# Optimization experiments

Hardware: AMD Instinct MI355X
Metric: run time of the kernel (lower is better)

Reference implementation:

```python
import jax, jax.numpy as jnp
import numpy as np

B, S, D = 2, 2048, 2048
H = 16
NOPE, ROPE, VDIM = 128, 64, 128
QKD = NOPE + ROPE  # 192
KV_RANK = 512
EPS = 1e-6
SCALE = QKD ** -0.5  # rope_factor <= 1.0 -> no mscale correction


def _rotate_half(x):
    h = x.shape[-1] // 2
    return jnp.concatenate([-x[..., h:], x[..., :h]], axis=-1)


def _rms_norm(x, w):
    var = jnp.mean(jnp.square(x), axis=-1, keepdims=True)
    return x * jax.lax.rsqrt(var + EPS) * w


def setup_inputs() -> dict:
    key = jax.random.key(0)
    ks = jax.random.split(key, 8)
    hidden_states = jax.random.normal(ks[0], (B, S, D), dtype=jnp.float32)
    cos = jax.random.uniform(ks[1], (S, ROPE), dtype=jnp.float32)
    sin = jax.random.uniform(ks[2], (S, ROPE), dtype=jnp.float32)
    # parameters (torch Linear stores [out, in]; keep same layout)
    wq_w = jax.random.normal(ks[3], (H * QKD, D), dtype=jnp.float32) * (D ** -0.5)
    wkv_a_w = jax.random.normal(ks[4], (KV_RANK + ROPE, D), dtype=jnp.float32) * (D ** -0.5)
    kv_norm_w = jnp.ones((KV_RANK,), dtype=jnp.float32)
    wkv_b_w = jax.random.normal(ks[5], (H * (NOPE + VDIM), KV_RANK), dtype=jnp.float32) * (KV_RANK ** -0.5)
    wo_w = jax.random.normal(ks[6], (D, H * VDIM), dtype=jnp.float32) * ((H * VDIM) ** -0.5)
    return dict(hidden_states=hidden_states, cos=cos, sin=sin,
                wq_w=wq_w, wkv_a_w=wkv_a_w, kv_norm_w=kv_norm_w,
                wkv_b_w=wkv_b_w, wo_w=wo_w)


def reference(hidden_states, cos, sin, wq_w, wkv_a_w, kv_norm_w, wkv_b_w, wo_w):
    x = hidden_states
    # q projection (q_lora_rank == 0 path)
    q = jnp.einsum('bsd,od->bso', x, wq_w).reshape(B, S, H, QKD)
    q_nope, q_pe = q[..., :NOPE], q[..., NOPE:]
    # low-rank kv
    kv_all = jnp.einsum('bsd,od->bso', x, wkv_a_w)  # [B,S,KV_RANK+ROPE]
    kv, k_pe = kv_all[..., :KV_RANK], kv_all[..., KV_RANK:]
    kv_proj = jnp.einsum('bsr,or->bso', _rms_norm(kv, kv_norm_w), wkv_b_w)
    kv_proj = kv_proj.reshape(B, S, H, NOPE + VDIM)
    k_nope, v = kv_proj[..., :NOPE], kv_proj[..., NOPE:]
    # rotary on pe parts; k_pe broadcast over heads
    c = cos[None, :, None, :]  # [1,S,1,ROPE]
    s = sin[None, :, None, :]
    q_pe = q_pe * c + _rotate_half(q_pe) * s
    k_pe_h = k_pe[:, :, None, :]  # broadcast over heads
    k_pe_h = k_pe_h * c + _rotate_half(k_pe_h) * s
    k_pe_h = jnp.broadcast_to(k_pe_h, (B, S, H, ROPE))
    k = jnp.concatenate([k_nope, k_pe_h], axis=-1)  # [B,S,H,QKD]
    qf = jnp.concatenate([q_nope, q_pe], axis=-1)
    # naive attention, fp32 softmax
    scores = jnp.einsum('bshd,bthd->bsht', qf, k) * SCALE
    attn = jax.nn.softmax(scores.astype(jnp.float32), axis=-1).astype(x.dtype)
    out = jnp.einsum('bsht,bthd->bshd', attn, v).reshape(B, S, H * VDIM)
    return jnp.einsum('bsf,of->bso', out, wo_w)
```

## Files before the change

kernel.cpp:

```cpp
#include <hip/hip_runtime.h>
#include <cstdint>


typedef _Float16 f16;
typedef _Float16 f16x8 __attribute__((ext_vector_type(8)));
typedef _Float16 f16x4 __attribute__((ext_vector_type(4)));
typedef float    f32x4 __attribute__((ext_vector_type(4)));

#define SCALE_L2E 0.104117550f

__device__ __forceinline__ void gl2lds16(const void* g, void* lds_wave_base) {
  __builtin_amdgcn_global_load_lds(
      (const __attribute__((address_space(1))) uint32_t*)(uintptr_t)g,
      (__attribute__((address_space(3))) uint32_t*)(uint32_t)(uintptr_t)lds_wave_base,
      16, 0, 0);
}

__global__ __launch_bounds__(256) void k_cvt(
    const float* __restrict__ x, const float* __restrict__ wq,
    const float* __restrict__ wkvb, const float* __restrict__ wo,
    const float* __restrict__ wkva,
    f16* __restrict__ xb, f16* __restrict__ wqb,
    f16* __restrict__ wkvbb, f16* __restrict__ wob,
    f16* __restrict__ wkvab)
{
  size_t i = ((size_t)blockIdx.x * 256 + threadIdx.x) * 4;
  if (i >= 20971520ull) {
    size_t il = i - 20971520ull;
    int r = (int)(il >> 11);
    f16x4 h;
    if (r < 576) {
      float4 v = *(const float4*)(wkva + il);
      h[0]=(f16)v.x; h[1]=(f16)v.y; h[2]=(f16)v.z; h[3]=(f16)v.w;
    } else { h[0]=h[1]=h[2]=h[3]=(f16)0.f; }
    *(f16x4*)(wkvab + il) = h;
    return;
  }
  const float* src; f16* dst; size_t off; float scl = 1.0f;
  if (i < 8388608ull)            { src = x;    dst = xb;    off = i; }
  else if (i < 14680064ull)      { src = wq;   dst = wqb;   off = i - 8388608ull; scl = SCALE_L2E; }
  else if (i < 16777216ull)      { src = wkvb; dst = wkvbb; off = i - 14680064ull; }
  else                           { src = wo;   dst = wob;   off = i - 16777216ull; }
  float4 v = *(const float4*)(src + off);
  f16x4 h; h[0]=(f16)(v.x*scl); h[1]=(f16)(v.y*scl); h[2]=(f16)(v.z*scl); h[3]=(f16)(v.w*scl);
  *(f16x4*)(dst + off) = h;
}

template<class Epi>
__device__ __forceinline__ void gemm256_core(const f16* __restrict__ Ablk,
                                             const f16* __restrict__ Bblk,
                                             int K, Epi epi)
{
  __shared__ __align__(16) f16 As[2][256 * 64];
  __shared__ __align__(16) f16 Bs[2][256 * 64];

  const int tid  = threadIdx.x;
  const int lane = tid & 63;
  const int wv   = tid >> 6;
  const int wm   = (wv >> 2) * 128;
  const int wn   = (wv & 3) * 64;
  const int lrow = lane & 15;
  const int lk   = lane >> 4;

  f32x4 acc[8][4];
#pragma unroll
  for (int i = 0; i < 8; ++i)
#pragma unroll
    for (int j = 0; j < 4; ++j) acc[i][j] = f32x4{0.f, 0.f, 0.f, 0.f};

  const int NT = K >> 6;

  const f16* aptr[4]; const f16* bptr[4]; int ldsbase[4];
#pragma unroll
  for (int q = 0; q < 4; ++q) {
    int s = q * 512 + tid;
    int r = s >> 3, c = s & 7;
    int gc = c ^ (r & 7);
    aptr[q] = Ablk + (size_t)r * K + gc * 8;
    bptr[q] = Bblk + (size_t)r * K + gc * 8;
    ldsbase[q] = (q * 512 + wv * 64) * 8;
  }

#pragma unroll
  for (int q = 0; q < 4; ++q) gl2lds16(aptr[q], (f16*)As[0] + ldsbase[q]);
#pragma unroll
  for (int q = 0; q < 4; ++q) gl2lds16(bptr[q], (f16*)Bs[0] + ldsbase[q]);

  for (int t = 0; t < NT; ++t) {
    const int cur = t & 1;
    asm volatile("s_waitcnt vmcnt(0)" ::: "memory");
    __builtin_amdgcn_s_barrier();
    const f16* Ac = As[cur];
    const f16* Bc = Bs[cur];
    const bool more = (t + 1 < NT);
    const int koff = (t + 1) * 64;
#pragma unroll
    for (int p = 0; p < 4; ++p) {
      if (p == 0 && more) {
#pragma unroll
        for (int q = 0; q < 4; ++q)
          gl2lds16(aptr[q] + koff, (f16*)As[cur ^ 1] + ldsbase[q]);
      }
      if (p == 1 && more) {
#pragma unroll
        for (int q = 0; q < 4; ++q)
          gl2lds16(bptr[q] + koff, (f16*)Bs[cur ^ 1] + ldsbase[q]);
      }
      const int mh = p >> 1, nh = p & 1;
      f16x8 af[2][4], bf[2][2];
#pragma unroll
      for (int ks = 0; ks < 2; ++ks) {
#pragma unroll
        for (int i = 0; i < 4; ++i) {
          int ra = wm + mh * 64 + i * 16 + lrow;
          int ca = (ks * 4 + lk) ^ (ra & 7);
          af[ks][i] = *(const f16x8*)(Ac + ra * 64 + ca * 8);
        }
#pragma unroll
        for (int j = 0; j < 2; ++j) {
          int rb = wn + nh * 32 + j * 16 + lrow;
          int cb = (ks * 4 + lk) ^ (rb & 7);
          bf[ks][j] = *(const f16x8*)(Bc + rb * 64 + cb * 8);
        }
      }
      __builtin_amdgcn_s_barrier();
      __builtin_amdgcn_s_setprio(1);
#pragma unroll
      for (int ks = 0; ks < 2; ++ks)
#pragma unroll
        for (int i = 0; i < 4; ++i)
#pragma unroll
          for (int j = 0; j < 2; ++j)
            acc[mh * 4 + i][nh * 2 + j] = __builtin_amdgcn_mfma_f32_16x16x32_f16(
                af[ks][i], bf[ks][j], acc[mh * 4 + i][nh * 2 + j], 0, 0, 0);
      __builtin_amdgcn_s_setprio(0);
      if (p < 3) __builtin_amdgcn_s_barrier();
    }
  }
  epi(acc, wm, wn, lk, lrow);
}

__global__ __launch_bounds__(512, 2) void k_gemm_qkva(
    const f16* __restrict__ xb, const f16* __restrict__ wqb,
    const f16* __restrict__ wkvab, const float* __restrict__ cosb,
    const float* __restrict__ sinb,
    f16* __restrict__ qraw, f16* __restrict__ kva)
{
  int nb = blockIdx.x, m0 = blockIdx.y * 256;
  bool isq = nb < 12;
  const f16* Bblk = isq ? wqb + (size_t)nb * 256 * 2048
                        : wkvab + (size_t)(nb - 12) * 256 * 2048;
  gemm256_core(xb + (size_t)m0 * 2048, Bblk, 2048,
    [&](f32x4 (&acc)[8][4], int wm, int wn, int lk, int lrow) {
      if (isq) {
        f16* Cb = qraw + (size_t)m0 * 3072 + nb * 256;
        int g = nb * 4 + (wn >> 6);
        if (g % 3 == 2) {
#pragma unroll
          for (int I = 0; I < 8; ++I)
#pragma unroll
            for (int rr = 0; rr < 4; ++rr) {
              int row = wm + I * 16 + lk * 4 + rr;
              int s = (m0 + row) & 2047;
              const float* cbp = cosb + (size_t)s * 64;
              const float* sbp = sinb + (size_t)s * 64;
#pragma unroll
              for (int J = 0; J < 4; ++J) {
                int tt = J * 16 + lrow;
                float v  = acc[I][J][rr];
                float pr = acc[I][J ^ 2][rr];
                float o = (J < 2) ? (v * cbp[tt] - pr * sbp[tt])
                                  : (v * cbp[tt] + pr * sbp[tt]);
                Cb[(size_t)row * 3072 + wn + J * 16 + lrow] = (f16)o;
              }
            }
          return;
        }
#pragma unroll
        for (int I = 0; I < 8; ++I)
#pragma unroll
          for (int rr = 0; rr < 4; ++rr) {
            int row = wm + I * 16 + lk * 4 + rr;
#pragma unroll
            for (int J = 0; J < 4; ++J)
              Cb[(size_t)row * 3072 + wn + J * 16 + lrow] = (f16)acc[I][J][rr];
          }
      } else {
        int n0k = (nb - 12) * 256;
        if (n0k + wn >= 640) return;
        f16* Cb = kva + (size_t)m0 * 640 + n0k;
#pragma unroll
        for (int I = 0; I < 8; ++I)
#pragma unroll
          for (int rr = 0; rr < 4; ++rr) {
            int row = wm + I * 16 + lk * 4 + rr;
#pragma unroll
            for (int J = 0; J < 4; ++J)
              Cb[(size_t)row * 640 + wn + J * 16 + lrow] = (f16)acc[I][J][rr];
          }
      }
    });
}

__global__ __launch_bounds__(512, 2) void k_gemm_kvb(
    const f16* __restrict__ kvn, const f16* __restrict__ wkvbb,
    f16* __restrict__ knope, f16* __restrict__ vf)
{
  int hh = blockIdx.x, m0 = blockIdx.y * 256;
  gemm256_core(kvn + (size_t)m0 * 512, wkvbb + (size_t)hh * 256 * 512, 512,
    [&](f32x4 (&acc)[8][4], int wm, int wn, int lk, int lrow) {
      if (wn >= 128) {
#pragma unroll
        for (int I = 0; I < 8; ++I) {
          int trow = m0 + wm + I * 16 + lk * 4;
          int bb = trow >> 11, ss = trow & 2047;
#pragma unroll
          for (int J = 0; J < 4; ++J) {
            int vd = (wn - 128) + J * 16 + lrow;
            f16x4 pk;
#pragma unroll
            for (int rr = 0; rr < 4; ++rr) pk[rr] = (f16)acc[I][J][rr];
            *(f16x4*)(vf + ((size_t)(bb * 16 + hh) * 128 + vd) * 2048 + ss) = pk;
          }
        }
      } else {
#pragma unroll
        for (int I = 0; I < 8; ++I)
#pragma unroll
          for (int rr = 0; rr < 4; ++rr) {
            int trow = m0 + wm + I * 16 + lk * 4 + rr;
#pragma unroll
            for (int J = 0; J < 4; ++J)
              knope[(size_t)trow * 2048 + hh * 128 + wn + J * 16 + lrow] = (f16)acc[I][J][rr];
          }
      }
    });
}

template<class Epi>
__device__ __forceinline__ void gemm_core(const f16* __restrict__ Ablk,
                                          const f16* __restrict__ Bblk,
                                          int K, Epi epi)
{
  __shared__ __align__(16) f16 As[128 * 64];
  __shared__ __align__(16) f16 Bs[128 * 64];

  const int tid  = threadIdx.x;
  const int lane = tid & 63;
  const int wv   = tid >> 6;
  const int wm = (wv >> 1) * 64, wn = (wv & 1) * 64;
  const int lrow = lane & 15;
  const int lk   = lane >> 4;

  f32x4 acc[4][4];
#pragma unroll
  for (int i = 0; i < 4; ++i)
#pragma unroll
    for (int j = 0; j < 4; ++j) acc[i][j] = f32x4{0.f, 0.f, 0.f, 0.f};

  for (int k0 = 0; k0 < K; k0 += 64) {
    __syncthreads();
#pragma unroll
    for (int it = 0; it < 4; ++it) {
      int s  = it * 256 + tid;
      int r  = s >> 3, sc = s & 7;
      int gc = sc ^ (r & 7);
      gl2lds16(Ablk + (size_t)r * K + k0 + gc * 8, (f16*)As + (size_t)(it * 256 + wv * 64) * 8);
      gl2lds16(Bblk + (size_t)r * K + k0 + gc * 8, (f16*)Bs + (size_t)(it * 256 + wv * 64) * 8);
    }
    __syncthreads();

#pragma unroll
    for (int ks = 0; ks < 2; ++ks) {
      f16x8 af[4], bf[4];
#pragma unroll
      for (int i = 0; i < 4; ++i) {
        int ra = wm + i * 16 + lrow;
        int ca = (ks * 4 + lk) ^ (ra & 7);
        af[i] = *(const f16x8*)(As + ra * 64 + ca * 8);
        int rb = wn + i * 16 + lrow;
        int cb = (ks * 4 + lk) ^ (rb & 7);
        bf[i] = *(const f16x8*)(Bs + rb * 64 + cb * 8);
      }
#pragma unroll
      for (int i = 0; i < 4; ++i)
#pragma unroll
        for (int j = 0; j < 4; ++j)
          acc[i][j] = __builtin_amdgcn_mfma_f32_16x16x32_f16(af[i], bf[j], acc[i][j], 0, 0, 0);
    }
  }
  epi(acc, wm, wn, lk, lrow);
}

__global__ __launch_bounds__(256, 3) void k_gemm_out(
    const f16* __restrict__ aout, const f16* __restrict__ wob, float* __restrict__ out)
{
  int n0 = blockIdx.x * 128, m0 = blockIdx.y * 128;
  gemm_core(aout + (size_t)m0 * 2048, wob + (size_t)n0 * 2048, 2048,
    [&](f32x4 (&acc)[4][4], int wm, int wn, int lk, int lrow) {
#pragma unroll
      for (int i = 0; i < 4; ++i)
#pragma unroll
        for (int rr = 0; rr < 4; ++rr) {
          int row = m0 + wm + i * 16 + lk * 4 + rr;
#pragma unroll
          for (int j = 0; j < 4; ++j)
            out[(size_t)row * 2048 + n0 + wn + j * 16 + lrow] = acc[i][j][rr];
        }
    });
}

__global__ __launch_bounds__(256) void k_rmsnorm_rope(
    const f16* __restrict__ kva, const float* __restrict__ w,
    const float* __restrict__ cosb, const float* __restrict__ sinb,
    f16* __restrict__ kvn, f16* __restrict__ kper)
{
  int row = blockIdx.x;
  int s = row & 2047;
  const f16* in = kva + (size_t)row * 640;
  int t = threadIdx.x;
  float v0 = (float)in[t], v1 = (float)in[t + 256];
  float ss = v0 * v0 + v1 * v1;
#pragma unroll
  for (int m = 1; m < 64; m <<= 1) ss += __shfl_xor(ss, m);
  __shared__ float red[4];
  if ((t & 63) == 0) red[t >> 6] = ss;
  __syncthreads();
  float tot = red[0] + red[1] + red[2] + red[3];
  float sc = rsqrtf(tot * (1.0f / 512.0f) + 1e-6f);
  kvn[(size_t)row * 512 + t]       = (f16)(v0 * sc * w[t]);
  kvn[(size_t)row * 512 + t + 256] = (f16)(v1 * sc * w[t + 256]);
  if (t < 32) {
    float a = (float)in[512 + t], bq = (float)in[512 + t + 32];
    float c0 = cosb[s * 64 + t], s0 = sinb[s * 64 + t];
    float c1 = cosb[s * 64 + t + 32], s1 = sinb[s * 64 + t + 32];
    kper[(size_t)row * 64 + t]      = (f16)(a * c0 - bq * s0);
    kper[(size_t)row * 64 + t + 32] = (f16)(bq * c1 + a * s1);
  }
}

#define PSTR 84

__global__ __launch_bounds__(512, 2) void k_attn(
    const f16* __restrict__ qraw, const f16* __restrict__ knope,
    const f16* __restrict__ kper, const f16* __restrict__ vf,
    f16* __restrict__ aout)
{
  int linear = blockIdx.x;
  int xcd  = linear & 7;
  int slot = linear >> 3;
  int hb   = (xcd << 2) | (slot & 3);
  int qt   = slot >> 2;
  int h = hb & 15, b = hb >> 4;
  int q0 = qt * 256;
  int tid = threadIdx.x, lane = tid & 63, wv = tid >> 6;
  int lrow = lane & 15, lk = lane >> 4;

  __shared__ __align__(16) f16 Ks[2][64 * 192];
  __shared__ __align__(16) f16 Vs[2][128 * 64];
  __shared__ __align__(16) f16 Ps[8][32 * PSTR];

  f16x8 qfr[2][6];
#pragma unroll
  for (int m = 0; m < 2; ++m) {
    const f16* qb = qraw + ((size_t)(b * 2048 + q0 + wv * 32 + m * 16 + lrow)) * 3072
                    + h * 192 + lk * 8;
#pragma unroll
    for (int ks = 0; ks < 6; ++ks) qfr[m][ks] = *(const f16x8*)(qb + ks * 32);
  }

  f32x4 oacc[2][8];
#pragma unroll
  for (int m = 0; m < 2; ++m)
#pragma unroll
    for (int i = 0; i < 8; ++i) oacc[m][i] = f32x4{0.f, 0.f, 0.f, 0.f};
  float l_st[2][4];
#pragma unroll
  for (int m = 0; m < 2; ++m)
#pragma unroll
    for (int r = 0; r < 4; ++r) l_st[m][r] = 0.f;

  const f16* knb = knope + ((size_t)b * 2048) * 2048 + h * 128;
  const f16* kpb = kper + (size_t)b * 2048 * 64;
  const f16* vb_ = vf + ((size_t)(b * 16 + h)) * 128 * 2048;

  const char* kp_ptr[3]; int kp_step[3];
#pragma unroll
  for (int it = 0; it < 3; ++it) {
    int s = it * 512 + tid;
    int r = s / 24, c = s - r * 24;
    int gc = c ^ (r & 7);
    if (gc < 16) { kp_ptr[it] = (const char*)(knb + (size_t)r * 2048 + gc * 8); kp_step[it] = 64 * 2048 * 2; }
    else         { kp_ptr[it] = (const char*)(kpb + (size_t)r * 64 + (gc - 16) * 8); kp_step[it] = 64 * 64 * 2; }
  }
  const char* vp_ptr[2];
#pragma unroll
  for (int it = 0; it < 2; ++it) {
    int s = it * 512 + tid;
    int r = s >> 3, c = s & 7, gc = c ^ (r & 7);
    vp_ptr[it] = (const char*)(vb_ + (size_t)r * 2048 + gc * 8);
  }

#pragma unroll
  for (int it = 0; it < 3; ++it) {
    gl2lds16(kp_ptr[it], (f16*)Ks[0] + (size_t)(it * 512 + wv * 64) * 8);
    kp_ptr[it] += kp_step[it];
  }
#pragma unroll
  for (int it = 0; it < 2; ++it) {
    gl2lds16(vp_ptr[it], (f16*)Vs[0] + (size_t)(it * 512 + wv * 64) * 8);
    vp_ptr[it] += 64 * 2;
  }

  int cur = 0;
  for (int t0 = 0; t0 < 2048; t0 += 64) {
    __syncthreads();
    if (t0 + 64 < 2048) {
#pragma unroll
      for (int it = 0; it < 3; ++it) {
        gl2lds16(kp_ptr[it], (f16*)Ks[cur ^ 1] + (size_t)(it * 512 + wv * 64) * 8);
        kp_ptr[it] += kp_step[it];
      }
#pragma unroll
      for (int it = 0; it < 2; ++it) {
        gl2lds16(vp_ptr[it], (f16*)Vs[cur ^ 1] + (size_t)(it * 512 + wv * 64) * 8);
        vp_ptr[it] += 64 * 2;
      }
    }
    const f16* Kc = Ks[cur];
    const f16* Vc = Vs[cur];

    f32x4 sacc[2][4];
#pragma unroll
    for (int m = 0; m < 2; ++m)
#pragma unroll
      for (int nt = 0; nt < 4; ++nt) sacc[m][nt] = f32x4{0.f, 0.f, 0.f, 0.f};
    __builtin_amdgcn_s_setprio(1);
#pragma unroll
    for (int nt = 0; nt < 4; ++nt) {
      int rb = nt * 16 + lrow;
#pragma unroll
      for (int ks = 0; ks < 6; ++ks) {
        int cc = (ks * 4 + lk) ^ (rb & 7);
        f16x8 bfr = *(const f16x8*)(Kc + rb * 192 + cc * 8);
        sacc[0][nt] = __builtin_amdgcn_mfma_f32_16x16x32_f16(qfr[0][ks], bfr, sacc[0][nt], 0, 0, 0);
        sacc[1][nt] = __builtin_amdgcn_mfma_f32_16x16x32_f16(qfr[1][ks], bfr, sacc[1][nt], 0, 0, 0);
      }
    }
    __builtin_amdgcn_s_setprio(0);

#pragma unroll
    for (int m = 0; m < 2; ++m) {
#pragma unroll
      for (int r = 0; r < 4; ++r) {
        float p0 = __builtin_amdgcn_exp2f(sacc[m][0][r]);
        float p1 = __builtin_amdgcn_exp2f(sacc[m][1][r]);
        float p2 = __builtin_amdgcn_exp2f(sacc[m][2][r]);
        float p3 = __builtin_amdgcn_exp2f(sacc[m][3][r]);
        l_st[m][r] += (p0 + p1) + (p2 + p3);
        int prow = (m * 16 + lk * 4 + r) * PSTR;
        Ps[wv][prow + 0 * 16 + lrow] = (f16)p0;
        Ps[wv][prow + 1 * 16 + lrow] = (f16)p1;
        Ps[wv][prow + 2 * 16 + lrow] = (f16)p2;
        Ps[wv][prow + 3 * 16 + lrow] = (f16)p3;
      }
    }
    __builtin_amdgcn_s_waitcnt(0xC07F);

    __builtin_amdgcn_s_setprio(1);
#pragma unroll
    for (int ks2 = 0; ks2 < 2; ++ks2) {
      f16x8 pa0 = *(const f16x8*)(&Ps[wv][(0 * 16 + lrow) * PSTR + ks2 * 32 + lk * 8]);
      f16x8 pa1 = *(const f16x8*)(&Ps[wv][(1 * 16 + lrow) * PSTR + ks2 * 32 + lk * 8]);
#pragma unroll
      for (int nv = 0; nv < 8; ++nv) {
        int rv = nv * 16 + lrow;
        int cc = (ks2 * 4 + lk) ^ (rv & 7);
        f16x8 vbf = *(const f16x8*)(Vc + rv * 64 + cc * 8);
        oacc[0][nv] = __builtin_amdgcn_mfma_f32_16x16x32_f16(pa0, vbf, oacc[0][nv], 0, 0, 0);
        oacc[1][nv] = __builtin_amdgcn_mfma_f32_16x16x32_f16(pa1, vbf, oacc[1][nv], 0, 0, 0);
      }
    }
    __builtin_amdgcn_s_setprio(0);
    cur ^= 1;
  }

  float rinv[2][4];
#pragma unroll
  for (int m = 0; m < 2; ++m)
#pragma unroll
    for (int r = 0; r < 4; ++r) {
      float l = l_st[m][r];
#pragma unroll
      for (int msk = 1; msk < 16; msk <<= 1) l += __shfl_xor(l, msk);
      rinv[m][r] = 1.0f / l;
    }
#pragma unroll
  for (int m = 0; m < 2; ++m) {
    f16* ob = aout + ((size_t)(b * 2048 + q0 + wv * 32 + m * 16 + lk * 4)) * 2048
              + h * 128 + lrow;
#pragma unroll
    for (int nv = 0; nv < 8; ++nv)
#pragma unroll
      for (int rr = 0; rr < 4; ++rr)
        ob[(size_t)rr * 2048 + nv * 16] = (f16)(oacc[m][nv][rr] * rinv[m][rr]);
  }
}

extern "C" void kernel_launch(void* const* d_in, const int* in_sizes, int n_in,
                              void* d_out, int out_size, void* d_ws, size_t ws_size,
                              hipStream_t stream)
{
  const float* x    = (const float*)d_in[0];
  const float* cosb = (const float*)d_in[1];
  const float* sinb = (const float*)d_in[2];
  const float* wq   = (const float*)d_in[3];
  const float* wkva = (const float*)d_in[4];
  const float* knw  = (const float*)d_in[5];
  const float* wkvb = (const float*)d_in[6];
  const float* wo   = (const float*)d_in[7];
  float* out = (float*)d_out;

  char* p = (char*)d_ws;
  auto take = [&](size_t elems) { char* r = p; p += (elems * 2 + 255) & ~(size_t)255; return r; };
  f16* xb    = (f16*)take(8388608ull);
  f16* wqb   = (f16*)take(6291456ull);
  f16* wkvab = (f16*)take(1572864ull);
  f16* wkvbb = (f16*)take(2097152ull);
  f16* wob   = (f16*)take(4194304ull);
  f16* qraw  = (f16*)take(12582912ull);
  f16* kva   = (f16*)take(2621440ull);
  f16* kvn   = (f16*)take(2097152ull);
  f16* kper  = (f16*)take(262144ull);
  f16* knope = (f16*)take(8388608ull);
  f16* vf    = (f16*)take(8388608ull);
  f16* aout  = (f16*)take(8388608ull);

  k_cvt<<<22016, 256, 0, stream>>>(x, wq, wkvb, wo, wkva, xb, wqb, wkvbb, wob, wkvab);
  k_gemm_qkva<<<dim3(15, 16), 512, 0, stream>>>(xb, wqb, wkvab, cosb, sinb, qraw, kva);
  k_rmsnorm_rope<<<4096, 256, 0, stream>>>(kva, knw, cosb, sinb, kvn, kper);
  k_gemm_kvb<<<dim3(16, 16), 512, 0, stream>>>(kvn, wkvbb, knope, vf);
  k_attn<<<dim3(256), 512, 0, stream>>>(qraw, knope, kper, vf, aout);
  k_gemm_out<<<dim3(16, 32), 256, 0, stream>>>(aout, wob, out);
}
```

Measured before the change: 364.4 us.

## Pipeline GEMM tile loads with partial vmcnt waits and remap blocks across XCDs

The shared 256x256 GEMM core now issues next-tile global-to-LDS loads in pieces ordered to match the four compute phases. It waits only on the specific outstanding loads each phase needs, with vmcnt(4/6/2/0), instead of draining all loads at the top of every K step. This removes one barrier per phase and is meant to overlap memory with MFMA work. Separately, the qkva and kvb GEMM kernels remap block indices with an idx&7 stride so that blocks landing on the same XCD share A/B tiles in L2. The risk is that the hand-counted vmcnt values are subtle, and any mismatch with the actual load ordering would cause a race.

```diff
diff --git a/kernel.cpp b/kernel.cpp
--- a/kernel.cpp
+++ b/kernel.cpp
@@ -70,72 +70,101 @@
 
   const int NT = K >> 6;
 
-  const f16* aptr[4]; const f16* bptr[4]; int ldsbase[4];
+  int s0A[4], s0B[4];
+  s0A[0] = tid;        s0A[1] = 1024 + tid;
+  s0A[2] = 512 + tid;  s0A[3] = 1536 + tid;
+  if (wv < 4) { s0B[0] = tid;       s0B[1] = 1024 + tid;
+                s0B[2] = 256 + tid; s0B[3] = 1280 + tid; }
+  else        { s0B[0] = 256 + tid; s0B[1] = 1280 + tid;
+                s0B[2] = 512 + tid; s0B[3] = 1536 + tid; }
+  const f16* ap[4]; const f16* bp[4]; int alb[4], blb[4];
 #pragma unroll
   for (int q = 0; q < 4; ++q) {
-    int s = q * 512 + tid;
-    int r = s >> 3, c = s & 7;
-    int gc = c ^ (r & 7);
-    aptr[q] = Ablk + (size_t)r * K + gc * 8;
-    bptr[q] = Bblk + (size_t)r * K + gc * 8;
-    ldsbase[q] = (q * 512 + wv * 64) * 8;
-  }
-
-#pragma unroll
-  for (int q = 0; q < 4; ++q) gl2lds16(aptr[q], (f16*)As[0] + ldsbase[q]);
-#pragma unroll
-  for (int q = 0; q < 4; ++q) gl2lds16(bptr[q], (f16*)Bs[0] + ldsbase[q]);
+    int rA = s0A[q] >> 3, cA = s0A[q] & 7, gA = cA ^ (rA & 7);
+    ap[q]  = Ablk + (size_t)rA * K + gA * 8;
+    alb[q] = (s0A[q] - lane) * 8;
+    int rB = s0B[q] >> 3, cB = s0B[q] & 7, gB = cB ^ (rB & 7);
+    bp[q]  = Bblk + (size_t)rB * K + gB * 8;
+    blb[q] = (s0B[q] - lane) * 8;
+  }
+
+  gl2lds16(bp[0], (f16*)Bs[0] + blb[0]);
+  gl2lds16(bp[1], (f16*)Bs[0] + blb[1]);
+  gl2lds16(ap[0], (f16*)As[0] + alb[0]);
+  gl2lds16(ap[1], (f16*)As[0] + alb[1]);
+  gl2lds16(bp[2], (f16*)Bs[0] + blb[2]);
+  gl2lds16(bp[3], (f16*)Bs[0] + blb[3]);
+  gl2lds16(ap[2], (f16*)As[0] + alb[2]);
+  gl2lds16(ap[3], (f16*)As[0] + alb[3]);
+
+  auto phase = [&](const f16* Ac, const f16* Bc, int mh, int nh) {
+    f16x8 af[2][4], bf[2][2];
+#pragma unroll
+    for (int ks = 0; ks < 2; ++ks) {
+#pragma unroll
+      for (int i = 0; i < 4; ++i) {
+        int ra = wm + mh * 64 + i * 16 + lrow;
+        int ca = (ks * 4 + lk) ^ (ra & 7);
+        af[ks][i] = *(const f16x8*)(Ac + ra * 64 + ca * 8);
+      }
+#pragma unroll
+      for (int j = 0; j < 2; ++j) {
+        int rb = wn + nh * 32 + j * 16 + lrow;
+        int cb = (ks * 4 + lk) ^ (rb & 7);
+        bf[ks][j] = *(const f16x8*)(Bc + rb * 64 + cb * 8);
+      }
+    }
+    __builtin_amdgcn_s_setprio(1);
+#pragma unroll
+    for (int ks = 0; ks < 2; ++ks)
+#pragma unroll
+      for (int i = 0; i < 4; ++i)
+#pragma unroll
+        for (int j = 0; j < 2; ++j)
+          acc[mh * 4 + i][nh * 2 + j] = __builtin_amdgcn_mfma_f32_16x16x32_f16(
+              af[ks][i], bf[ks][j], acc[mh * 4 + i][nh * 2 + j], 0, 0, 0);
+    __builtin_amdgcn_s_setprio(0);
+  };
 
   for (int t = 0; t < NT; ++t) {
-    const int cur = t & 1;
-    asm volatile("s_waitcnt vmcnt(0)" ::: "memory");
-    __builtin_amdgcn_s_barrier();
-    const f16* Ac = As[cur];
-    const f16* Bc = Bs[cur];
+    const int buf = t & 1;
+    const f16* Ac = As[buf];
+    const f16* Bc = Bs[buf];
+    f16* An = (f16*)As[buf ^ 1];
+    f16* Bn = (f16*)Bs[buf ^ 1];
     const bool more = (t + 1 < NT);
     const int koff = (t + 1) * 64;
-#pragma unroll
-    for (int p = 0; p < 4; ++p) {
-      if (p == 0 && more) {
-#pragma unroll
-        for (int q = 0; q < 4; ++q)
-          gl2lds16(aptr[q] + koff, (f16*)As[cur ^ 1] + ldsbase[q]);
-      }
-      if (p == 1 && more) {
-#pragma unroll
-        for (int q = 0; q < 4; ++q)
-          gl2lds16(bptr[q] + koff, (f16*)Bs[cur ^ 1] + ldsbase[q]);
-      }
-      const int mh = p >> 1, nh = p & 1;
-      f16x8 af[2][4], bf[2][2];
-#pragma unroll
-      for (int ks = 0; ks < 2; ++ks) {
-#pragma unroll
-        for (int i = 0; i < 4; ++i) {
-          int ra = wm + mh * 64 + i * 16 + lrow;
-          int ca = (ks * 4 + lk) ^ (ra & 7);
-          af[ks][i] = *(const f16x8*)(Ac + ra * 64 + ca * 8);
-        }
-#pragma unroll
-        for (int j = 0; j < 2; ++j) {
-          int rb = wn + nh * 32 + j * 16 + lrow;
-          int cb = (ks * 4 + lk) ^ (rb & 7);
-          bf[ks][j] = *(const f16x8*)(Bc + rb * 64 + cb * 8);
-        }
-      }
-      __builtin_amdgcn_s_barrier();
-      __builtin_amdgcn_s_setprio(1);
-#pragma unroll
-      for (int ks = 0; ks < 2; ++ks)
-#pragma unroll
-        for (int i = 0; i < 4; ++i)
-#pragma unroll
-          for (int j = 0; j < 2; ++j)
-            acc[mh * 4 + i][nh * 2 + j] = __builtin_amdgcn_mfma_f32_16x16x32_f16(
-                af[ks][i], bf[ks][j], acc[mh * 4 + i][nh * 2 + j], 0, 0, 0);
-      __builtin_amdgcn_s_setprio(0);
-      if (p < 3) __builtin_amdgcn_s_barrier();
-    }
+
+    asm volatile("s_waitcnt vmcnt(4)" ::: "memory");
+    __builtin_amdgcn_s_barrier();
+    if (more) {
+      gl2lds16(bp[0] + koff, Bn + blb[0]);
+      gl2lds16(bp[1] + koff, Bn + blb[1]);
+      gl2lds16(ap[0] + koff, An + alb[0]);
+      gl2lds16(ap[1] + koff, An + alb[1]);
+    }
+    phase(Ac, Bc, 0, 0);
+
+    if (more) asm volatile("s_waitcnt vmcnt(6)" ::: "memory");
+    else      asm volatile("s_waitcnt vmcnt(2)" ::: "memory");
+    __builtin_amdgcn_s_barrier();
+    if (more) {
+      gl2lds16(bp[2] + koff, Bn + blb[2]);
+      gl2lds16(bp[3] + koff, Bn + blb[3]);
+    }
+    phase(Ac, Bc, 0, 1);
+
+    if (more) asm volatile("s_waitcnt vmcnt(6)" ::: "memory");
+    else      asm volatile("s_waitcnt vmcnt(0)" ::: "memory");
+    __builtin_amdgcn_s_barrier();
+    if (more) {
+      gl2lds16(ap[2] + koff, An + alb[2]);
+      gl2lds16(ap[3] + koff, An + alb[3]);
+    }
+    phase(Ac, Bc, 1, 0);
+
+    __builtin_amdgcn_s_barrier();
+    phase(Ac, Bc, 1, 1);
   }
   epi(acc, wm, wn, lk, lrow);
 }
@@ -146,7 +175,9 @@
     const float* __restrict__ sinb,
     f16* __restrict__ qraw, f16* __restrict__ kva)
 {
-  int nb = blockIdx.x, m0 = blockIdx.y * 256;
+  int idx  = blockIdx.y * 15 + blockIdx.x;
+  int nidx = (idx & 7) * 30 + (idx >> 3);
+  int nb = nidx % 15, m0 = (nidx / 15) * 256;
   bool isq = nb < 12;
   const f16* Bblk = isq ? wqb + (size_t)nb * 256 * 2048
                         : wkvab + (size_t)(nb - 12) * 256 * 2048;
@@ -206,7 +237,9 @@
     const f16* __restrict__ kvn, const f16* __restrict__ wkvbb,
     f16* __restrict__ knope, f16* __restrict__ vf)
 {
-  int hh = blockIdx.x, m0 = blockIdx.y * 256;
+  int idx  = blockIdx.y * 16 + blockIdx.x;
+  int nidx = (idx & 7) * 32 + (idx >> 3);
+  int hh = nidx & 15, m0 = (nidx >> 4) * 256;
   gemm256_core(kvn + (size_t)m0 * 512, wkvbb + (size_t)hh * 256 * 512, 512,
     [&](f32x4 (&acc)[8][4], int wm, int wn, int lk, int lrow) {
       if (wn >= 128) {
```

Result: no change. 359.5 us (-1.4%).
